# Optimization experiments

Hardware: AMD Instinct MI355X
Metric: run time of the kernel (lower is better)

Reference implementation:

```python
import jax, jax.numpy as jnp
import numpy as np

B, S, D = 2, 2048, 2048
H, G = 32, 8          # num_heads, num_kv_groups
GS = H // G           # group_size = 4
HD = D // H           # head_dim = 64


def setup_inputs() -> dict:
    key = jax.random.key(0)
    ks = jax.random.split(key, 5)
    x = jax.random.normal(ks[0], (B, S, D), dtype=jnp.float32)
    Wq = jax.random.normal(ks[1], (D, D), dtype=jnp.float32) * 0.02
    Wk = jax.random.normal(ks[2], (G * HD, D), dtype=jnp.float32) * 0.02
    Wv = jax.random.normal(ks[3], (G * HD, D), dtype=jnp.float32) * 0.02
    Wo = jax.random.normal(ks[4], (D, D), dtype=jnp.float32) * 0.02
    return {"x": x, "Wq": Wq, "Wk": Wk, "Wv": Wv, "Wo": Wo}


def reference(x, Wq, Wk, Wv, Wo):
    b, s, _ = x.shape
    # Projections (nn.Linear: x @ W.T, no bias)
    # queries: view(b,s,H,HD) with head h = g*GS + j -> reshape to (b,s,G,GS,HD)
    q = (x @ Wq.T).reshape(b, s, G, GS, HD)
    k = (x @ Wk.T).reshape(b, s, G, HD)   # [b, s, G, HD]
    v = (x @ Wv.T).reshape(b, s, G, HD)
    # repeat_interleave(group_size, dim=heads): head h uses kv group h // GS,
    # which is exactly the grouped einsum below (no materialized repeat).
    scores = jnp.einsum('bqgjd,bkgd->bgjqk', q, k) / np.sqrt(HD).astype(np.float32)
    # prefill cache: ptr=0, so mask is plain causal (q_pos < k_pos masked out)
    qpos = jnp.arange(s)
    mask = qpos[:, None] < qpos[None, :]        # [s, s], True = masked
    scores = jnp.where(mask, -jnp.inf, scores)
    w = jax.nn.softmax(scores, axis=-1)         # dropout p=0.0 (eval)
    ctx = jnp.einsum('bgjqk,bkgd->bqgjd', w, v).reshape(b, s, D)
    return ctx @ Wo.T
```

## Files before the change

kernel.cpp:

```cpp
#include <hip/hip_runtime.h>
#include <hip/hip_bf16.h>

typedef unsigned short u16;
typedef short bf16x8 __attribute__((ext_vector_type(8)));
typedef float f32x4 __attribute__((ext_vector_type(4)));

#define NEG_BIG (-1e30f)
#define SCL 0.18033688f

__device__ __forceinline__ u16 f2bf(float f) {
    union { float f; unsigned int u; } x; x.f = f;
    unsigned int r = x.u + 0x7fffu + ((x.u >> 16) & 1u);
    return (u16)(r >> 16);
}

__device__ __forceinline__ void dma16(const u16* g, const u16* lds) {
    __builtin_amdgcn_global_load_lds(
        (const __attribute__((address_space(1))) unsigned int*)g,
        (__attribute__((address_space(3))) unsigned int*)lds, 16, 0, 0);
}

__device__ __forceinline__ bf16x8 sfrag(const u16* lds, int row, int kb8) {
    int slot = row * 8 + (kb8 ^ (row & 7));
    return *(const bf16x8*)(lds + slot * 8);
}

__global__ __launch_bounds__(256) void cvt_all(const float* __restrict__ x,
                                               const float* __restrict__ wq,
                                               const float* __restrict__ wk,
                                               const float* __restrict__ wv,
                                               const float* __restrict__ wo,
                                               u16* __restrict__ xb, u16* __restrict__ wqb,
                                               u16* __restrict__ wkb, u16* __restrict__ wvb,
                                               u16* __restrict__ wob) {
    size_t i = (size_t)blockIdx.x * 256 + threadIdx.x;
    const float* s; u16* d; size_t off;
    if      (i < 1048576) { s = x;  d = xb;  off = i; }
    else if (i < 1572864) { s = wq; d = wqb; off = i - 1048576; }
    else if (i < 1703936) { s = wk; d = wkb; off = i - 1572864; }
    else if (i < 1835008) { s = wv; d = wvb; off = i - 1703936; }
    else                  { s = wo; d = wob; off = i - 1835008; }
    const float* p = s + off * 8;
    float4 a = *(const float4*)p;
    float4 b = *(const float4*)(p + 4);
    bf16x8 r;
    r[0] = (short)f2bf(a.x); r[1] = (short)f2bf(a.y);
    r[2] = (short)f2bf(a.z); r[3] = (short)f2bf(a.w);
    r[4] = (short)f2bf(b.x); r[5] = (short)f2bf(b.y);
    r[6] = (short)f2bf(b.z); r[7] = (short)f2bf(b.w);
    *(bf16x8*)(d + off * 8) = r;
}

__global__ __launch_bounds__(256) void gemm_bt(const u16* __restrict__ A,
                                               const u16* __restrict__ Bt,
                                               float* __restrict__ C,
                                               int M, int N, int K) {
    __shared__ u16 As[8192];
    __shared__ u16 Bs[8192];
    const int t = threadIdx.x;
    const int wave = t >> 6, lane = t & 63;
    const int wm = (wave >> 1) * 64, wn = (wave & 1) * 64;
    const int lhi = lane >> 4, llo = lane & 15;
    const int m0 = blockIdx.y * 128, n0 = blockIdx.x * 128;
    const int wbase = wave * 64;

    f32x4 acc[4][4] = {};
    for (int k0 = 0; k0 < K; k0 += 64) {
        const u16* Ab = A + (size_t)m0 * K + k0;
        const u16* Bb = Bt + (size_t)n0 * K + k0;
#pragma unroll
        for (int i = 0; i < 4; ++i) {
            int s = i * 256 + t;
            int row = s >> 3, gch = (s & 7) ^ (row & 7);
            dma16(Ab + (size_t)row * K + gch * 8, As + (i * 256 + wbase) * 8);
            dma16(Bb + (size_t)row * K + gch * 8, Bs + (i * 256 + wbase) * 8);
        }
        __syncthreads();
#pragma unroll
        for (int ks = 0; ks < 2; ++ks) {
            const int kb = ks * 4 + lhi;
            bf16x8 af[4], bfg[4];
#pragma unroll
            for (int mi = 0; mi < 4; ++mi) af[mi] = sfrag(As, wm + mi * 16 + llo, kb);
#pragma unroll
            for (int ni = 0; ni < 4; ++ni) bfg[ni] = sfrag(Bs, wn + ni * 16 + llo, kb);
#pragma unroll
            for (int mi = 0; mi < 4; ++mi)
#pragma unroll
                for (int ni = 0; ni < 4; ++ni)
                    acc[mi][ni] = __builtin_amdgcn_mfma_f32_16x16x32_bf16(
                        af[mi], bfg[ni], acc[mi][ni], 0, 0, 0);
        }
        __syncthreads();
    }
#pragma unroll
    for (int mi = 0; mi < 4; ++mi)
#pragma unroll
        for (int ni = 0; ni < 4; ++ni)
#pragma unroll
            for (int r = 0; r < 4; ++r) {
                int row = m0 + wm + mi * 16 + lhi * 4 + r;
                int col = n0 + wn + ni * 16 + llo;
                C[(size_t)row * N + col] = acc[mi][ni][r];
            }
}

__global__ __launch_bounds__(256) void gemm_qkv(const u16* __restrict__ A,
                                                const u16* __restrict__ Wq,
                                                const u16* __restrict__ Wk,
                                                const u16* __restrict__ Wv,
                                                u16* __restrict__ Qout,
                                                u16* __restrict__ Kout,
                                                u16* __restrict__ Vtout) {
    const int K = 2048;
    __shared__ u16 As[8192];
    __shared__ u16 Bs[8192];
    const int t = threadIdx.x;
    const int wave = t >> 6, lane = t & 63;
    const int wm = (wave >> 1) * 64, wn = (wave & 1) * 64;
    const int lhi = lane >> 4, llo = lane & 15;
    const int m0 = blockIdx.y * 128;
    const int bx = blockIdx.x;
    const int kind = (bx < 16) ? 0 : (bx < 20 ? 1 : 2);
    const int n0 = (kind == 0) ? bx * 128 : (bx & 3) * 128;
    const u16* Bt = ((kind == 0) ? Wq : (kind == 1) ? Wk : Wv) + (size_t)n0 * K;
    const int wbase = wave * 64;

    f32x4 acc[4][4] = {};
    for (int k0 = 0; k0 < K; k0 += 64) {
        const u16* Ab = A + (size_t)m0 * K + k0;
        const u16* Bb = Bt + k0;
#pragma unroll
        for (int i = 0; i < 4; ++i) {
            int s = i * 256 + t;
            int row = s >> 3, gch = (s & 7) ^ (row & 7);
            dma16(Ab + (size_t)row * K + gch * 8, As + (i * 256 + wbase) * 8);
            dma16(Bb + (size_t)row * K + gch * 8, Bs + (i * 256 + wbase) * 8);
        }
        __syncthreads();
#pragma unroll
        for (int ks = 0; ks < 2; ++ks) {
            const int kb = ks * 4 + lhi;
            bf16x8 af[4], bfg[4];
#pragma unroll
            for (int mi = 0; mi < 4; ++mi) af[mi] = sfrag(As, wm + mi * 16 + llo, kb);
#pragma unroll
            for (int ni = 0; ni < 4; ++ni) bfg[ni] = sfrag(Bs, wn + ni * 16 + llo, kb);
#pragma unroll
            for (int mi = 0; mi < 4; ++mi)
#pragma unroll
                for (int ni = 0; ni < 4; ++ni)
                    acc[mi][ni] = __builtin_amdgcn_mfma_f32_16x16x32_bf16(
                        af[mi], bfg[ni], acc[mi][ni], 0, 0, 0);
        }
        __syncthreads();
    }

    if (kind == 0) {
#pragma unroll
        for (int mi = 0; mi < 4; ++mi)
#pragma unroll
            for (int ni = 0; ni < 4; ++ni)
#pragma unroll
                for (int r = 0; r < 4; ++r) {
                    int row = m0 + wm + mi * 16 + lhi * 4 + r;
                    int col = n0 + wn + ni * 16 + llo;
                    Qout[(size_t)row * 2048 + col] = f2bf(acc[mi][ni][r] * SCL);
                }
    } else if (kind == 1) {
#pragma unroll
        for (int mi = 0; mi < 4; ++mi)
#pragma unroll
            for (int ni = 0; ni < 4; ++ni)
#pragma unroll
                for (int r = 0; r < 4; ++r) {
                    int row = m0 + wm + mi * 16 + lhi * 4 + r;
                    int col = n0 + wn + ni * 16 + llo;
                    Kout[(size_t)row * 512 + col] = f2bf(acc[mi][ni][r]);
                }
    } else {
#pragma unroll
        for (int mi = 0; mi < 4; ++mi)
#pragma unroll
            for (int ni = 0; ni < 4; ++ni) {
                int row = m0 + wm + mi * 16 + lhi * 4;
                int col = n0 + wn + ni * 16 + llo;
                size_t off = ((size_t)col + (size_t)(row >> 11) * 512) * 2048 + (row & 2047);
                short4 v;
                v.x = (short)f2bf(acc[mi][ni][0]);
                v.y = (short)f2bf(acc[mi][ni][1]);
                v.z = (short)f2bf(acc[mi][ni][2]);
                v.w = (short)f2bf(acc[mi][ni][3]);
                *(short4*)(Vtout + off) = v;
            }
    }
}

__global__ __launch_bounds__(256, 4) void attn5(const u16* __restrict__ Q,
                                                const u16* __restrict__ Kb,
                                                const u16* __restrict__ Vt,
                                                u16* __restrict__ Ctx) {
    __shared__ u16 Ks[4096];
    __shared__ u16 Vs[4096];
    __shared__ u16 Pl[4][16][72];
    const int bg = blockIdx.y;
    const int b = bg >> 3, g = bg & 7;
    const int t = threadIdx.x, w = t >> 6, lane = t & 63;
    const int lhi = lane >> 4, llo = lane & 15;
    const int h = g * 4 + w;
    const int wbase = w * 64;

    const u16* Kp = Kb + (size_t)(b * 2048) * 512 + g * 64;
    const u16* Vp = Vt + (size_t)bg * 64 * 2048;

#pragma unroll
    for (int ph = 0; ph < 2; ++ph) {
        const int qt = ph ? (int)blockIdx.x : 127 - (int)blockIdx.x;

        const u16* Qp = Q + ((size_t)(b * 2048 + qt * 16)) * 2048 + h * 64;
        bf16x8 aq[2];
#pragma unroll
        for (int ks = 0; ks < 2; ++ks)
            aq[ks] = *(const bf16x8*)(Qp + (size_t)llo * 2048 + ks * 32 + lhi * 8);

        f32x4 o[4] = {};
        float m_ = NEG_BIG, l_ = 0.f;

        const int ktmax = (qt * 16 + 15) >> 6;
        for (int kt = 0; kt <= ktmax; ++kt) {
            __syncthreads();
#pragma unroll
            for (int i = 0; i < 2; ++i) {
                int s = i * 256 + t;
                int row = s >> 3, gch = (s & 7) ^ (row & 7);
                dma16(Kp + (size_t)(kt * 64 + row) * 512 + gch * 8, Ks + (i * 256 + wbase) * 8);
                dma16(Vp + (size_t)row * 2048 + (size_t)kt * 64 + gch * 8, Vs + (i * 256 + wbase) * 8);
            }
            __syncthreads();

            f32x4 st[4] = {};
#pragma unroll
            for (int ks = 0; ks < 2; ++ks) {
                const int kb8 = ks * 4 + lhi;
                bf16x8 kf[4];
#pragma unroll
                for (int kb = 0; kb < 4; ++kb) kf[kb] = sfrag(Ks, kb * 16 + llo, kb8);
#pragma unroll
                for (int kb = 0; kb < 4; ++kb)
                    st[kb] = __builtin_amdgcn_mfma_f32_16x16x32_bf16(
                        kf[kb], aq[ks], st[kb], 0, 0, 0);
            }

            if (kt * 64 + 63 > qt * 16) {
                int qg = qt * 16 + llo;
#pragma unroll
                for (int kb = 0; kb < 4; ++kb)
#pragma unroll
                    for (int r = 0; r < 4; ++r) {
                        int kg = kt * 64 + kb * 16 + lhi * 4 + r;
                        if (kg > qg) st[kb][r] = NEG_BIG;
                    }
            }

            float mx = st[0][0];
#pragma unroll
            for (int kb = 0; kb < 4; ++kb)
#pragma unroll
                for (int r = 0; r < 4; ++r) mx = fmaxf(mx, st[kb][r]);
            mx = fmaxf(mx, __shfl_xor(mx, 16, 64));
            mx = fmaxf(mx, __shfl_xor(mx, 32, 64));
            float mn = fmaxf(m_, mx);
            float alpha = exp2f(m_ - mn);
            m_ = mn;
            float rsum = 0.f;

#pragma unroll
            for (int kb = 0; kb < 4; ++kb) {
                float p0 = exp2f(st[kb][0] - m_);
                float p1 = exp2f(st[kb][1] - m_);
                float p2 = exp2f(st[kb][2] - m_);
                float p3 = exp2f(st[kb][3] - m_);
                rsum += (p0 + p1) + (p2 + p3);
                short4 pk;
                pk.x = (short)f2bf(p0); pk.y = (short)f2bf(p1);
                pk.z = (short)f2bf(p2); pk.w = (short)f2bf(p3);
                *(short4*)(&Pl[w][llo][kb * 16 + lhi * 4]) = pk;
            }
            rsum += __shfl_xor(rsum, 16, 64);
            rsum += __shfl_xor(rsum, 32, 64);
            l_ = l_ * alpha + rsum;
#pragma unroll
            for (int hb = 0; hb < 4; ++hb)
#pragma unroll
                for (int r = 0; r < 4; ++r) o[hb][r] *= alpha;

            __builtin_amdgcn_s_waitcnt(0xC07F);

#pragma unroll
            for (int ks2 = 0; ks2 < 2; ++ks2) {
                bf16x8 pf = *(const bf16x8*)(&Pl[w][llo][ks2 * 32 + lhi * 8]);
                bf16x8 vf[4];
#pragma unroll
                for (int hb = 0; hb < 4; ++hb) vf[hb] = sfrag(Vs, hb * 16 + llo, ks2 * 4 + lhi);
#pragma unroll
                for (int hb = 0; hb < 4; ++hb)
                    o[hb] = __builtin_amdgcn_mfma_f32_16x16x32_bf16(
                        vf[hb], pf, o[hb], 0, 0, 0);
            }
        }

        u16* Cp = Ctx + (size_t)(b * 2048 + qt * 16) * 2048 + h * 64;
        float inv = 1.0f / l_;
#pragma unroll
        for (int hb = 0; hb < 4; ++hb) {
            short4 v;
            v.x = (short)f2bf(o[hb][0] * inv);
            v.y = (short)f2bf(o[hb][1] * inv);
            v.z = (short)f2bf(o[hb][2] * inv);
            v.w = (short)f2bf(o[hb][3] * inv);
            *(short4*)(Cp + (size_t)llo * 2048 + hb * 16 + lhi * 4) = v;
        }
    }
}

extern "C" void kernel_launch(void* const* d_in, const int* in_sizes, int n_in,
                              void* d_out, int out_size, void* d_ws, size_t ws_size,
                              hipStream_t stream) {
    const float* x  = (const float*)d_in[0];
    const float* Wq = (const float*)d_in[1];
    const float* Wk = (const float*)d_in[2];
    const float* Wv = (const float*)d_in[3];
    const float* Wo = (const float*)d_in[4];

    u16* xb  = (u16*)d_ws;
    u16* wqb = xb + 8388608;
    u16* wkb = wqb + 4194304;
    u16* wvb = wkb + 1048576;
    u16* wob = wvb + 1048576;
    u16* Kb  = wob + 4194304;
    u16* Vtb = Kb + 2097152;
    u16* Ctx = xb;
    u16* Qb  = (u16*)d_out;
    float* out = (float*)d_out;

    cvt_all<<<dim3(9216), 256, 0, stream>>>(x, Wq, Wk, Wv, Wo, xb, wqb, wkb, wvb, wob);
    gemm_qkv<<<dim3(24, 32), 256, 0, stream>>>(xb, wqb, wkb, wvb, Qb, Kb, Vtb);
    attn5<<<dim3(64, 16), 256, 0, stream>>>(Qb, Kb, Vtb, Ctx);
    gemm_bt<<<dim3(16, 32), 256, 0, stream>>>(Ctx, wob, out, 4096, 2048, 2048);
}
```

Measured before the change: 316.4 us.

## Double-buffer K/V tiles and keep P in registers in attention

Result: faster. 307.9 us (median of 2 runs) (-2.7%).

```diff
diff --git a/kernel.cpp b/kernel.cpp
--- a/kernel.cpp
+++ b/kernel.cpp
@@ -2,6 +2,7 @@
 #include <hip/hip_bf16.h>
 
 typedef unsigned short u16;
+typedef short bf16x4 __attribute__((ext_vector_type(4)));
 typedef short bf16x8 __attribute__((ext_vector_type(8)));
 typedef float f32x4 __attribute__((ext_vector_type(4)));
 
@@ -14,6 +15,21 @@
     return (u16)(r >> 16);
 }
 
+__device__ __forceinline__ unsigned cvtpk(float lo, float hi) {
+    unsigned r;
+    asm("v_cvt_pk_bf16_f32 %0, %1, %2" : "=v"(r) : "v"(lo), "v"(hi));
+    return r;
+}
+
+__device__ __forceinline__ f32x4 mfma16(bf16x4 a, bf16x4 b, f32x4 c) {
+#if __has_builtin(__builtin_amdgcn_mfma_f32_16x16x16bf16_1k)
+    return __builtin_amdgcn_mfma_f32_16x16x16bf16_1k(a, b, c, 0, 0, 0);
+#else
+    asm("v_mfma_f32_16x16x16_bf16 %0, %1, %2, %0" : "+v"(c) : "v"(a), "v"(b));
+    return c;
+#endif
+}
+
 __device__ __forceinline__ void dma16(const u16* g, const u16* lds) {
     __builtin_amdgcn_global_load_lds(
         (const __attribute__((address_space(1))) unsigned int*)g,
@@ -23,6 +39,12 @@
 __device__ __forceinline__ bf16x8 sfrag(const u16* lds, int row, int kb8) {
     int slot = row * 8 + (kb8 ^ (row & 7));
     return *(const bf16x8*)(lds + slot * 8);
+}
+
+__device__ __forceinline__ bf16x4 vfrag(const u16* lds, int row, int kb, int lhi) {
+    int c = kb * 2 + (lhi >> 1);
+    int slot = row * 8 + (c ^ (row & 7));
+    return *(const bf16x4*)(lds + slot * 8 + (lhi & 1) * 4);
 }
 
 __global__ __launch_bounds__(256) void cvt_all(const float* __restrict__ x,
@@ -196,13 +218,12 @@
     }
 }
 
-__global__ __launch_bounds__(256, 4) void attn5(const u16* __restrict__ Q,
-                                                const u16* __restrict__ Kb,
-                                                const u16* __restrict__ Vt,
+__global__ __launch_bounds__(256, 4) void attn6(const u16* __restrict__ Q,
+                                                const u16* __restrict__ Kbuf,
+                                                const u16* __restrict__ Vtb,
                                                 u16* __restrict__ Ctx) {
-    __shared__ u16 Ks[4096];
-    __shared__ u16 Vs[4096];
-    __shared__ u16 Pl[4][16][72];
+    __shared__ u16 Ks[2][4096];
+    __shared__ u16 Vs[2][4096];
     const int bg = blockIdx.y;
     const int b = bg >> 3, g = bg & 7;
     const int t = threadIdx.x, w = t >> 6, lane = t & 63;
@@ -210,8 +231,24 @@
     const int h = g * 4 + w;
     const int wbase = w * 64;
 
-    const u16* Kp = Kb + (size_t)(b * 2048) * 512 + g * 64;
-    const u16* Vp = Vt + (size_t)bg * 64 * 2048;
+    const u16* Kp = Kbuf + (size_t)(b * 2048) * 512 + g * 64;
+    const u16* Vp = Vtb + (size_t)bg * 64 * 2048;
+
+    const int r0 = t >> 3,          g0 = (t & 7) ^ (r0 & 7);
+    const int r1 = (256 + t) >> 3,  g1 = ((256 + t) & 7) ^ (r1 & 7);
+
+    bf16x4 ones;
+    ones[0] = ones[1] = ones[2] = ones[3] = (short)0x3F80;
+
+    auto STAGE = [&](int kt, int bufi) {
+        const u16* Kt = Kp + (size_t)kt * 64 * 512;
+        const u16* Vt2 = Vp + kt * 64;
+        u16* Kd = Ks[bufi]; u16* Vd = Vs[bufi];
+        dma16(Kt + (size_t)r0 * 512 + g0 * 8, Kd + wbase * 8);
+        dma16(Vt2 + (size_t)r0 * 2048 + g0 * 8, Vd + wbase * 8);
+        dma16(Kt + (size_t)r1 * 512 + g1 * 8, Kd + (256 + wbase) * 8);
+        dma16(Vt2 + (size_t)r1 * 2048 + g1 * 8, Vd + (256 + wbase) * 8);
+    };
 
 #pragma unroll
     for (int ph = 0; ph < 2; ++ph) {
@@ -224,32 +261,35 @@
             aq[ks] = *(const bf16x8*)(Qp + (size_t)llo * 2048 + ks * 32 + lhi * 8);
 
         f32x4 o[4] = {};
-        float m_ = NEG_BIG, l_ = 0.f;
+        f32x4 lac = {};
+        float m_ = NEG_BIG;
 
         const int ktmax = (qt * 16 + 15) >> 6;
+
+        STAGE(0, 0);
+        asm volatile("s_waitcnt vmcnt(0)" ::: "memory");
+        __builtin_amdgcn_s_barrier();
+
         for (int kt = 0; kt <= ktmax; ++kt) {
-            __syncthreads();
-#pragma unroll
-            for (int i = 0; i < 2; ++i) {
-                int s = i * 256 + t;
-                int row = s >> 3, gch = (s & 7) ^ (row & 7);
-                dma16(Kp + (size_t)(kt * 64 + row) * 512 + gch * 8, Ks + (i * 256 + wbase) * 8);
-                dma16(Vp + (size_t)row * 2048 + (size_t)kt * 64 + gch * 8, Vs + (i * 256 + wbase) * 8);
-            }
-            __syncthreads();
+            const int cur = kt & 1;
+            if (kt < ktmax) STAGE(kt + 1, cur ^ 1);
+            const u16* Ksb = Ks[cur];
+            const u16* Vsb = Vs[cur];
 
             f32x4 st[4] = {};
+            __builtin_amdgcn_s_setprio(1);
 #pragma unroll
             for (int ks = 0; ks < 2; ++ks) {
                 const int kb8 = ks * 4 + lhi;
                 bf16x8 kf[4];
 #pragma unroll
-                for (int kb = 0; kb < 4; ++kb) kf[kb] = sfrag(Ks, kb * 16 + llo, kb8);
+                for (int kb = 0; kb < 4; ++kb) kf[kb] = sfrag(Ksb, kb * 16 + llo, kb8);
 #pragma unroll
                 for (int kb = 0; kb < 4; ++kb)
                     st[kb] = __builtin_amdgcn_mfma_f32_16x16x32_bf16(
                         kf[kb], aq[ks], st[kb], 0, 0, 0);
             }
+            __builtin_amdgcn_s_setprio(0);
 
             if (kt * 64 + 63 > qt * 16) {
                 int qg = qt * 16 + llo;
@@ -262,63 +302,60 @@
                     }
             }
 
-            float mx = st[0][0];
-#pragma unroll
-            for (int kb = 0; kb < 4; ++kb)
-#pragma unroll
-                for (int r = 0; r < 4; ++r) mx = fmaxf(mx, st[kb][r]);
+            float t0 = fmaxf(fmaxf(st[0][0], st[0][1]), st[0][2]);
+            float t1 = fmaxf(fmaxf(st[0][3], st[1][0]), st[1][1]);
+            float t2 = fmaxf(fmaxf(st[1][2], st[1][3]), st[2][0]);
+            float t3 = fmaxf(fmaxf(st[2][1], st[2][2]), st[2][3]);
+            float t4 = fmaxf(fmaxf(st[3][0], st[3][1]), st[3][2]);
+            float mx = fmaxf(fmaxf(fmaxf(t0, t1), t2),
+                             fmaxf(fmaxf(t3, t4), st[3][3]));
             mx = fmaxf(mx, __shfl_xor(mx, 16, 64));
             mx = fmaxf(mx, __shfl_xor(mx, 32, 64));
-            float mn = fmaxf(m_, mx);
-            float alpha = exp2f(m_ - mn);
-            m_ = mn;
-            float rsum = 0.f;
-
+
+            if (__any(mx > m_ + 8.0f)) {
+                float mn = fmaxf(m_, mx);
+                float alpha = exp2f(m_ - mn);
+                m_ = mn;
+#pragma unroll
+                for (int hb = 0; hb < 4; ++hb) o[hb] *= alpha;
+                lac *= alpha;
+            }
+
+            bf16x4 pf[4];
 #pragma unroll
             for (int kb = 0; kb < 4; ++kb) {
                 float p0 = exp2f(st[kb][0] - m_);
                 float p1 = exp2f(st[kb][1] - m_);
                 float p2 = exp2f(st[kb][2] - m_);
                 float p3 = exp2f(st[kb][3] - m_);
-                rsum += (p0 + p1) + (p2 + p3);
-                short4 pk;
-                pk.x = (short)f2bf(p0); pk.y = (short)f2bf(p1);
-                pk.z = (short)f2bf(p2); pk.w = (short)f2bf(p3);
-                *(short4*)(&Pl[w][llo][kb * 16 + lhi * 4]) = pk;
-            }
-            rsum += __shfl_xor(rsum, 16, 64);
-            rsum += __shfl_xor(rsum, 32, 64);
-            l_ = l_ * alpha + rsum;
-#pragma unroll
-            for (int hb = 0; hb < 4; ++hb)
-#pragma unroll
-                for (int r = 0; r < 4; ++r) o[hb][r] *= alpha;
-
-            __builtin_amdgcn_s_waitcnt(0xC07F);
-
-#pragma unroll
-            for (int ks2 = 0; ks2 < 2; ++ks2) {
-                bf16x8 pf = *(const bf16x8*)(&Pl[w][llo][ks2 * 32 + lhi * 8]);
-                bf16x8 vf[4];
-#pragma unroll
-                for (int hb = 0; hb < 4; ++hb) vf[hb] = sfrag(Vs, hb * 16 + llo, ks2 * 4 + lhi);
+                union { unsigned u[2]; bf16x4 v; } pu;
+                pu.u[0] = cvtpk(p0, p1);
+                pu.u[1] = cvtpk(p2, p3);
+                pf[kb] = pu.v;
+            }
+
+            __builtin_amdgcn_s_setprio(1);
+#pragma unroll
+            for (int kb = 0; kb < 4; ++kb) lac = mfma16(ones, pf[kb], lac);
+#pragma unroll
+            for (int kb = 0; kb < 4; ++kb)
 #pragma unroll
                 for (int hb = 0; hb < 4; ++hb)
-                    o[hb] = __builtin_amdgcn_mfma_f32_16x16x32_bf16(
-                        vf[hb], pf, o[hb], 0, 0, 0);
-            }
-        }
-
+                    o[hb] = mfma16(vfrag(Vsb, hb * 16 + llo, kb, lhi), pf[kb], o[hb]);
+            __builtin_amdgcn_s_setprio(0);
+
+            asm volatile("s_waitcnt vmcnt(0)" ::: "memory");
+            __builtin_amdgcn_s_barrier();
+        }
+
+        float inv = 1.0f / lac[0];
         u16* Cp = Ctx + (size_t)(b * 2048 + qt * 16) * 2048 + h * 64;
-        float inv = 1.0f / l_;
 #pragma unroll
         for (int hb = 0; hb < 4; ++hb) {
-            short4 v;
-            v.x = (short)f2bf(o[hb][0] * inv);
-            v.y = (short)f2bf(o[hb][1] * inv);
-            v.z = (short)f2bf(o[hb][2] * inv);
-            v.w = (short)f2bf(o[hb][3] * inv);
-            *(short4*)(Cp + (size_t)llo * 2048 + hb * 16 + lhi * 4) = v;
+            union { unsigned u[2]; short4 s; } cu;
+            cu.u[0] = cvtpk(o[hb][0] * inv, o[hb][1] * inv);
+            cu.u[1] = cvtpk(o[hb][2] * inv, o[hb][3] * inv);
+            *(short4*)(Cp + (size_t)llo * 2048 + hb * 16 + lhi * 4) = cu.s;
         }
     }
 }
@@ -345,6 +382,6 @@
 
     cvt_all<<<dim3(9216), 256, 0, stream>>>(x, Wq, Wk, Wv, Wo, xb, wqb, wkb, wvb, wob);
     gemm_qkv<<<dim3(24, 32), 256, 0, stream>>>(xb, wqb, wkb, wvb, Qb, Kb, Vtb);
-    attn5<<<dim3(64, 16), 256, 0, stream>>>(Qb, Kb, Vtb, Ctx);
+    attn6<<<dim3(64, 16), 256, 0, stream>>>(Qb, Kb, Vtb, Ctx);
     gemm_bt<<<dim3(16, 32), 256, 0, stream>>>(Ctx, wob, out, 4096, 2048, 2048);
 }
```
